# Optimization experiments

Measured on AMD Instinct MI355X. Metric: run time of the kernel, lower is better.

## Reference

```python
import jax, jax.numpy as jnp
import numpy as np

EMBED = 1024
HEADS = 16
HEAD_DIM = EMBED // HEADS
SCALE = HEAD_DIM ** (-0.5)
LN_EPS = 1e-5


def setup_inputs() -> dict:
    key = jax.random.key(0)
    ks = jax.random.split(key, 8)
    B, N = 2, 2048
    s = EMBED ** -0.5
    return {
        "x": jax.random.normal(ks[0], (B, N, EMBED), dtype=jnp.float32),
        "ln_w": jnp.ones((EMBED,), jnp.float32),
        "ln_b": jnp.zeros((EMBED,), jnp.float32),
        "Wq": jax.random.normal(ks[1], (EMBED, EMBED), jnp.float32) * s,
        "Wk": jax.random.normal(ks[2], (EMBED, EMBED), jnp.float32) * s,
        "Wv": jax.random.normal(ks[3], (EMBED, EMBED), jnp.float32) * s,
        "Wo": jax.random.normal(ks[4], (EMBED, EMBED), jnp.float32) * s,
        "bo": jnp.zeros((EMBED,), jnp.float32),
    }


def reference(x, ln_w, ln_b, Wq, Wk, Wv, Wo, bo):
    residual = x
    # LayerNorm (pre-norm)
    mu = jnp.mean(x, axis=-1, keepdims=True)
    var = jnp.mean(jnp.square(x - mu), axis=-1, keepdims=True)
    xn = (x - mu) * jax.lax.rsqrt(var + LN_EPS) * ln_w + ln_b

    B, N, _ = xn.shape
    q = (xn @ Wq.T).reshape(B, N, HEADS, HEAD_DIM).transpose(0, 2, 1, 3)  # b h n d
    k = (xn @ Wk.T).reshape(B, N, HEADS, HEAD_DIM).transpose(0, 2, 1, 3)
    v = (xn @ Wv.T).reshape(B, N, HEADS, HEAD_DIM).transpose(0, 2, 1, 3)

    dots = jnp.einsum('bhqd,bhkd->bhqk', q, k) * SCALE
    causal = jnp.tril(jnp.ones((N, N), dtype=bool))
    dots = jnp.where(causal, dots, -jnp.inf)
    attn = jax.nn.softmax(dots, axis=-1)
    out = jnp.einsum('bhqk,bhkd->bhqd', attn, v)
    out = out.transpose(0, 2, 1, 3).reshape(B, N, EMBED)
    # dropout is identity in eval mode
    return residual + out @ Wo.T + bo
```

## Files before the change

### kernel.cpp

```cpp
#include <hip/hip_runtime.h>

#define E 1024
#define NSEQ 2048
#define HEADS 16
#define HD 64

typedef unsigned short u16;
typedef short short8 __attribute__((ext_vector_type(8)));
typedef float f32x4 __attribute__((ext_vector_type(4)));

template<bool B> struct BC { static constexpr bool v = B; };

#define GLOAD_LDS16(gp, lp)                                        \
    __builtin_amdgcn_global_load_lds(                              \
        (const __attribute__((address_space(1))) void*)(gp),       \
        (__attribute__((address_space(3))) void*)(lp), 16, 0, 0)

__device__ __forceinline__ u16 f2bf(float f) {
    union { float f; unsigned u; } v; v.f = f;
    unsigned r = v.u + 0x7fffu + ((v.u >> 16) & 1u);
    return (u16)(r >> 16);
}

__device__ __forceinline__ unsigned cvt_pk_bf16(float lo, float hi) {
    unsigned r;
    asm("v_cvt_pk_bf16_f32 %0, %1, %2" : "=v"(r) : "v"(lo), "v"(hi));
    return r;
}

__device__ __forceinline__ f32x4 mfma16(short8 a, short8 b, f32x4 c) {
    return __builtin_amdgcn_mfma_f32_16x16x32_bf16(a, b, c, 0, 0, 0);
}

__global__ __launch_bounds__(256) void convw_k(
    const float* __restrict__ Wq, const float* __restrict__ Wk,
    const float* __restrict__ Wv, const float* __restrict__ Wo,
    u16* __restrict__ out)
{
    const unsigned i = (blockIdx.x * 256u + threadIdx.x) * 4u;
    const unsigned m = i >> 20;
    const float* src = (m == 0) ? Wq : (m == 1) ? Wk : (m == 2) ? Wv : Wo;
    const float4 v = *(const float4*)(src + (i & 0xFFFFFu));
    *(uint2*)(out + i) = make_uint2(
        ((unsigned)f2bf(v.x)) | (((unsigned)f2bf(v.y)) << 16),
        ((unsigned)f2bf(v.z)) | (((unsigned)f2bf(v.w)) << 16));
}

__global__ __launch_bounds__(256) void ln_fwd(
    const float* __restrict__ X, const float* __restrict__ w,
    const float* __restrict__ bb, u16* __restrict__ xn)
{
    const int row = blockIdx.x, tid = threadIdx.x;
    const int lane = tid & 63, wave = tid >> 6;
    const float4 v = ((const float4*)(X + (size_t)row * E))[tid];
    float s = v.x + v.y + v.z + v.w;
    float s2 = v.x * v.x + v.y * v.y + v.z * v.z + v.w * v.w;
#pragma unroll
    for (int off = 1; off < 64; off <<= 1) {
        s += __shfl_xor(s, off);
        s2 += __shfl_xor(s2, off);
    }
    __shared__ float red[8];
    if (lane == 0) { red[wave] = s; red[4 + wave] = s2; }
    __syncthreads();
    s = red[0] + red[1] + red[2] + red[3];
    s2 = red[4] + red[5] + red[6] + red[7];
    const float mu = s * (1.f / 1024.f);
    float var = s2 * (1.f / 1024.f) - mu * mu;
    var = fmaxf(var, 0.f);
    const float rs = rsqrtf(var + 1e-5f);
    const float4 wv = ((const float4*)w)[tid];
    const float4 bv = ((const float4*)bb)[tid];
    u16 o0 = f2bf((v.x - mu) * rs * wv.x + bv.x);
    u16 o1 = f2bf((v.y - mu) * rs * wv.y + bv.y);
    u16 o2 = f2bf((v.z - mu) * rs * wv.z + bv.z);
    u16 o3 = f2bf((v.w - mu) * rs * wv.w + bv.w);
    *(uint2*)(xn + (size_t)row * E + tid * 4) =
        make_uint2(((unsigned)o0) | (((unsigned)o1) << 16),
                   ((unsigned)o2) | (((unsigned)o3) << 16));
}

__global__ __launch_bounds__(256) void vtrans(
    const u16* __restrict__ Vb, u16* __restrict__ VT)
{
    __shared__ u16 tl[64][65];
    const int t = threadIdx.x;
    const int ntile = blockIdx.x, bh = blockIdx.y;
    const int b = bh >> 4, h = bh & 15;
    const int n0 = ntile * 64;
    {
        const int nl = t >> 2;
        const u16* src = Vb + ((size_t)b * NSEQ + n0 + nl) * E + h * 64;
#pragma unroll
        for (int u = 0; u < 2; ++u) {
            const int d0 = (t & 3) * 16 + u * 8;
            short8 v = *(const short8*)(src + d0);
#pragma unroll
            for (int j = 0; j < 8; ++j) tl[nl][d0 + j] = (u16)v[j];
        }
    }
    __syncthreads();
    {
        const int d = t >> 2, nc = (t & 3) * 16;
        u16* dst = VT + ((size_t)bh * 64 + d) * NSEQ + n0 + nc;
#pragma unroll
        for (int u = 0; u < 2; ++u) {
            short8 o;
#pragma unroll
            for (int j = 0; j < 8; ++j) o[j] = (short)tl[nc + u * 8 + j][d];
            *(short8*)(dst + u * 8) = o;
        }
    }
}

template<int MODE>
__global__ __launch_bounds__(256) void gemm_nt(
    const u16* __restrict__ A, const u16* __restrict__ Wbase,
    u16* __restrict__ outb, float* __restrict__ outf,
    const float* __restrict__ resid, const float* __restrict__ bias)
{
    __shared__ __align__(16) unsigned char As[128 * 128];
    __shared__ __align__(16) unsigned char Bs[128 * 128];
    const int tid = threadIdx.x;
    const int lane = tid & 63, wave = tid >> 6;
    const int l15 = lane & 15, l4 = lane >> 4;
    const int wm = wave >> 1, wn = wave & 1;
    const int nt = blockIdx.x, mt = blockIdx.y, z = blockIdx.z;
    const u16* Bw = Wbase + (size_t)z * (E * (size_t)E);

    const int lrow8 = lane >> 3;
    const int lchunk = (lane & 7) ^ lrow8;
    const u16* gA = A + (size_t)(mt * 128 + lrow8) * E + lchunk * 8;
    const u16* gB = Bw + (size_t)(nt * 128 + lrow8) * E + lchunk * 8;

    f32x4 acc[4][4] = {};

    for (int kt = 0; kt < 16; ++kt) {
#pragma unroll
        for (int i = 0; i < 4; ++i) {
            const int rb = (i * 4 + wave) * 8;
            GLOAD_LDS16(gA + (size_t)rb * E + kt * 64, As + rb * 128);
            GLOAD_LDS16(gB + (size_t)rb * E + kt * 64, Bs + rb * 128);
        }
        __syncthreads();
#pragma unroll
        for (int ks = 0; ks < 2; ++ks) {
            short8 af[4], bfr[4];
#pragma unroll
            for (int i = 0; i < 4; ++i) {
                int ra = wm * 64 + i * 16 + l15;
                af[i] = *(const short8*)(As + ra * 128 + ((ks * 64 + l4 * 16) ^ ((ra & 7) << 4)));
                int rb2 = wn * 64 + i * 16 + l15;
                bfr[i] = *(const short8*)(Bs + rb2 * 128 + ((ks * 64 + l4 * 16) ^ ((rb2 & 7) << 4)));
            }
#pragma unroll
            for (int i = 0; i < 4; ++i)
#pragma unroll
                for (int j = 0; j < 4; ++j)
                    acc[i][j] = mfma16(af[i], bfr[j], acc[i][j]);
        }
        __syncthreads();
    }

    const int orow0 = mt * 128 + wm * 64, ocol0 = nt * 128 + wn * 64;
    if (MODE == 0) {
        u16* outz = outb + (size_t)z * (4096 * (size_t)E);
        const float osc = (z == 0) ? 0.18033688f : 1.0f;
#pragma unroll
        for (int i = 0; i < 4; ++i)
#pragma unroll
            for (int j = 0; j < 4; ++j)
#pragma unroll
                for (int r = 0; r < 4; ++r) {
                    int row = orow0 + i * 16 + l4 * 4 + r;
                    int col = ocol0 + j * 16 + l15;
                    outz[(size_t)row * E + col] = f2bf(acc[i][j][r] * osc);
                }
    } else {
#pragma unroll
        for (int i = 0; i < 4; ++i)
#pragma unroll
            for (int j = 0; j < 4; ++j)
#pragma unroll
                for (int r = 0; r < 4; ++r) {
                    int row = orow0 + i * 16 + l4 * 4 + r;
                    int col = ocol0 + j * 16 + l15;
                    size_t idx = (size_t)row * E + col;
                    outf[idx] = acc[i][j][r] + resid[idx] + bias[col];
                }
    }
}

__global__ __launch_bounds__(256) void attn_fwd(
    const u16* __restrict__ Q, const u16* __restrict__ K,
    const u16* __restrict__ VT, u16* __restrict__ O)
{
    __shared__ __align__(16) unsigned char Kls[2 * 16384];
    __shared__ __align__(16) unsigned char Vls[2 * 16384];
    __shared__ __align__(16) unsigned char Ps[4 * 4096];
    const int tid = threadIdx.x, lane = tid & 63, wave = tid >> 6;
    const int sub = wave >> 1, par = wave & 1;
    const int l15 = lane & 15, l4 = lane >> 4;
    const int h = blockIdx.x, j = blockIdx.y, b = blockIdx.z;
    const size_t bbase = (size_t)b * NSEQ * E + h * HD;
    const u16* vt = VT + ((size_t)(b * 16 + h) * 64) * NSEQ;

    unsigned char* Pw = Ps + wave * 4096;
    const int srowK = lane >> 3, kchunk = (lane & 7) ^ srowK;
    const int srowV = lane >> 4, vchunk = (lane & 15) ^ (((wave & 1) << 2) + srowV);

    auto stage = [&](int t, int buf) {
        const u16* Kg = K + bbase + (size_t)(t * 128) * E;
        const u16* vg = vt + t * 128;
        unsigned char* kd = Kls + buf * 16384 + wave * 1024;
        unsigned char* vd = Vls + buf * 16384 + wave * 1024;
#pragma unroll
        for (int i = 0; i < 4; ++i)
            GLOAD_LDS16(Kg + (size_t)(wave * 8 + i * 32 + srowK) * E + kchunk * 8, kd + i * 4096);
#pragma unroll
        for (int i = 0; i < 4; ++i)
            GLOAD_LDS16(vg + (size_t)(wave * 4 + i * 16 + srowV) * NSEQ + vchunk * 8, vd + i * 4096);
    };

    auto run_strip = [&](int jj) {
        const int qw0 = jj * 64 + sub * 32;
        const int R = (jj >> 1) + 1;

        short8 aq[2][2];
#pragma unroll
        for (int qt = 0; qt < 2; ++qt)
#pragma unroll
            for (int ks = 0; ks < 2; ++ks)
                aq[qt][ks] = *(const short8*)(Q + bbase + (size_t)(qw0 + qt * 16 + l15) * E + ks * 32 + l4 * 8);

        f32x4 accO[2][4] = {};
        float mrow[2] = {-5e29f, -5e29f};
        float lrow[2] = {0.f, 0.f};

        stage(0, 0);
        __syncthreads();

        auto step = [&](int t, auto mc) {
            constexpr bool MASK = decltype(mc)::v;
            const int buf = t & 1;
            if (t + 1 < R) stage(t + 1, buf ^ 1);
            const unsigned char* Kc = Kls + buf * 16384;
            const unsigned char* Vc = Vls + buf * 16384;

            f32x4 s[2][4] = {};
#pragma unroll
            for (int kvt = 0; kvt < 4; ++kvt) {
                const int kr = par * 64 + kvt * 16 + l15;
#pragma unroll
                for (int ks = 0; ks < 2; ++ks) {
                    short8 kfr = *(const short8*)(Kc + kr * 128 + ((ks * 64 + l4 * 16) ^ ((kr & 7) << 4)));
                    s[0][kvt] = mfma16(kfr, aq[0][ks], s[0][kvt]);
                    s[1][kvt] = mfma16(kfr, aq[1][ks], s[1][kvt]);
                }
            }

            if constexpr (MASK) {
#pragma unroll
                for (int qt = 0; qt < 2; ++qt) {
                    const int qg = qw0 + qt * 16 + l15;
#pragma unroll
                    for (int kvt = 0; kvt < 4; ++kvt)
#pragma unroll
                        for (int r = 0; r < 4; ++r) {
                            int kvg = t * 128 + par * 64 + kvt * 16 + l4 * 4 + r;
                            if (kvg > qg) s[qt][kvt][r] = -1e30f;
                        }
                }
            }

#pragma unroll
            for (int qt = 0; qt < 2; ++qt) {
                float m0 = fmaxf(fmaxf(s[qt][0][0], s[qt][0][1]), fmaxf(s[qt][0][2], s[qt][0][3]));
                float m1 = fmaxf(fmaxf(s[qt][1][0], s[qt][1][1]), fmaxf(s[qt][1][2], s[qt][1][3]));
                float m2 = fmaxf(fmaxf(s[qt][2][0], s[qt][2][1]), fmaxf(s[qt][2][2], s[qt][2][3]));
                float m3 = fmaxf(fmaxf(s[qt][3][0], s[qt][3][1]), fmaxf(s[qt][3][2], s[qt][3][3]));
                float pm = fmaxf(fmaxf(m0, m1), fmaxf(m2, m3));
                if (__any(pm > mrow[qt] + 8.f)) {
                    pm = fmaxf(pm, __shfl_xor(pm, 16));
                    pm = fmaxf(pm, __shfl_xor(pm, 32));
                    const float mn = fmaxf(mrow[qt], pm);
                    const float sc = exp2f(mrow[qt] - mn);
                    mrow[qt] = mn;
                    lrow[qt] *= sc;
#pragma unroll
                    for (int r = 0; r < 4; ++r) {
                        float scv = __shfl(sc, l4 * 4 + r);
#pragma unroll
                        for (int dt = 0; dt < 4; ++dt) accO[qt][dt][r] *= scv;
                    }
                }
                const int pr = qt * 16 + l15;
                const int sw = (l15 & 7) << 4;
#pragma unroll
                for (int kvt = 0; kvt < 4; ++kvt) {
                    float p0 = exp2f(s[qt][kvt][0] - mrow[qt]);
                    float p1 = exp2f(s[qt][kvt][1] - mrow[qt]);
                    float p2 = exp2f(s[qt][kvt][2] - mrow[qt]);
                    float p3 = exp2f(s[qt][kvt][3] - mrow[qt]);
                    lrow[qt] += (p0 + p1) + (p2 + p3);
                    uint2 pk = make_uint2(cvt_pk_bf16(p0, p1), cvt_pk_bf16(p2, p3));
                    *(uint2*)(Pw + pr * 128 + ((kvt * 32 + l4 * 8) ^ sw)) = pk;
                }
            }

#pragma unroll
            for (int ks2 = 0; ks2 < 2; ++ks2) {
                const int cb = ks2 * 64 + l4 * 16;
                short8 pf0 = *(const short8*)(Pw + l15 * 128 + (cb ^ ((l15 & 7) << 4)));
                short8 pf1 = *(const short8*)(Pw + (16 + l15) * 128 + (cb ^ ((l15 & 7) << 4)));
#pragma unroll
                for (int dt = 0; dt < 4; ++dt) {
                    const int vr = dt * 16 + l15;
                    short8 vfr = *(const short8*)(Vc + vr * 256 + ((par * 128 + cb) ^ ((vr & 7) << 4)));
                    accO[0][dt] = mfma16(pf0, vfr, accO[0][dt]);
                    accO[1][dt] = mfma16(pf1, vfr, accO[1][dt]);
                }
            }
            __syncthreads();
        };

        for (int t = 0; t + 1 < R; ++t) step(t, BC<false>{});
        step(R - 1, BC<true>{});

        f32x4* Mg = (f32x4*)Kls;
        if (par == 1) {
            f32x4 hd;
            hd[0] = mrow[0]; hd[1] = mrow[1]; hd[2] = lrow[0]; hd[3] = lrow[1];
            Mg[(sub * 9) * 64 + lane] = hd;
#pragma unroll
            for (int qt = 0; qt < 2; ++qt)
#pragma unroll
                for (int dt = 0; dt < 4; ++dt)
                    Mg[(sub * 9 + 1 + qt * 4 + dt) * 64 + lane] = accO[qt][dt];
        }
        __syncthreads();
        if (par == 0) {
            f32x4 hd = Mg[(sub * 9) * 64 + lane];
            float scA[2], scB[2];
#pragma unroll
            for (int qt = 0; qt < 2; ++qt) {
                const float mB = hd[qt], lB = hd[2 + qt];
                const float ms = fmaxf(mrow[qt], mB);
                scA[qt] = exp2f(mrow[qt] - ms);
                scB[qt] = exp2f(mB - ms);
                lrow[qt] = lrow[qt] * scA[qt] + lB * scB[qt];
            }
#pragma unroll
            for (int qt = 0; qt < 2; ++qt)
#pragma unroll
                for (int r = 0; r < 4; ++r) {
                    float sa = __shfl(scA[qt], l4 * 4 + r);
                    float sb = __shfl(scB[qt], l4 * 4 + r);
#pragma unroll
                    for (int dt = 0; dt < 4; ++dt) {
                        f32x4 ob = Mg[(sub * 9 + 1 + qt * 4 + dt) * 64 + lane];
                        accO[qt][dt][r] = accO[qt][dt][r] * sa + ob[r] * sb;
                    }
                }
            float linv[2];
#pragma unroll
            for (int qt = 0; qt < 2; ++qt) {
                float tl2 = lrow[qt];
                tl2 += __shfl_xor(tl2, 16);
                tl2 += __shfl_xor(tl2, 32);
                linv[qt] = 1.f / tl2;
            }
#pragma unroll
            for (int rt = 0; rt < 2; ++rt)
#pragma unroll
                for (int r = 0; r < 4; ++r) {
                    float lq = __shfl(linv[rt], l4 * 4 + r);
                    const int qg = qw0 + rt * 16 + l4 * 4 + r;
#pragma unroll
                    for (int dt = 0; dt < 4; ++dt)
                        O[bbase + (size_t)qg * E + dt * 16 + l15] = f2bf(accO[rt][dt][r] * lq);
                }
        }
        __syncthreads();
    };

    run_strip(j);
    run_strip(31 - j);
}

extern "C" void kernel_launch(void* const* d_in, const int* in_sizes, int n_in,
                              void* d_out, int out_size, void* d_ws, size_t ws_size,
                              hipStream_t stream)
{
    const float* x    = (const float*)d_in[0];
    const float* ln_w = (const float*)d_in[1];
    const float* ln_b = (const float*)d_in[2];
    const float* Wq   = (const float*)d_in[3];
    const float* Wk   = (const float*)d_in[4];
    const float* Wv   = (const float*)d_in[5];
    const float* Wo   = (const float*)d_in[6];
    const float* bo   = (const float*)d_in[7];
    float* out = (float*)d_out;

    u16* ws  = (u16*)d_ws;
    u16* Wbf = ws;
    u16* xn  = Wbf + (size_t)4 * 1024 * 1024;
    u16* Qb  = xn + (size_t)4096 * 1024;
    u16* Kb  = Qb + (size_t)4096 * 1024;
    u16* Vb  = Kb + (size_t)4096 * 1024;
    u16* Ob  = Vb + (size_t)4096 * 1024;
    u16* VT  = xn;

    convw_k<<<dim3(4096), dim3(256), 0, stream>>>(Wq, Wk, Wv, Wo, Wbf);
    ln_fwd<<<dim3(4096), dim3(256), 0, stream>>>(x, ln_w, ln_b, xn);
    gemm_nt<0><<<dim3(8, 32, 3), dim3(256), 0, stream>>>(
        xn, Wbf, Qb, nullptr, nullptr, nullptr);
    vtrans<<<dim3(32, 32), dim3(256), 0, stream>>>(Vb, VT);
    attn_fwd<<<dim3(16, 16, 2), dim3(256), 0, stream>>>(Qb, Kb, VT, Ob);
    gemm_nt<1><<<dim3(8, 32, 1), dim3(256), 0, stream>>>(
        Ob, Wbf + (size_t)3 * 1024 * 1024, nullptr, out, x, bo);
}
```

Baseline: 122.4 us.

## Load V fragments directly from global into registers, drop V LDS staging

The attention kernel no longer stages V^T tiles through shared memory. Each wave loads its own V fragments straight from global memory into registers, prefetching the next tile after the PV MFMAs. LDS address offsets are precomputed once per thread, and s_setprio is raised around the MFMA blocks. This halves LDS footprint and removes the V LDS traffic, but exposes global load latency on V loads that are only one step ahead, and adds register pressure.

```diff
diff --git a/kernel.cpp b/kernel.cpp
--- a/kernel.cpp
+++ b/kernel.cpp
@@ -196,30 +196,53 @@
     const u16* __restrict__ VT, u16* __restrict__ O)
 {
     __shared__ __align__(16) unsigned char Kls[2 * 16384];
-    __shared__ __align__(16) unsigned char Vls[2 * 16384];
     __shared__ __align__(16) unsigned char Ps[4 * 4096];
     const int tid = threadIdx.x, lane = tid & 63, wave = tid >> 6;
     const int sub = wave >> 1, par = wave & 1;
     const int l15 = lane & 15, l4 = lane >> 4;
-    const int h = blockIdx.x, j = blockIdx.y, b = blockIdx.z;
+    const int h = blockIdx.x, jg = blockIdx.y, b = blockIdx.z;
     const size_t bbase = (size_t)b * NSEQ * E + h * HD;
     const u16* vt = VT + ((size_t)(b * 16 + h) * 64) * NSEQ;
 
     unsigned char* Pw = Ps + wave * 4096;
     const int srowK = lane >> 3, kchunk = (lane & 7) ^ srowK;
-    const int srowV = lane >> 4, vchunk = (lane & 15) ^ (((wave & 1) << 2) + srowV);
+
+    int koff[4][2];
+#pragma unroll
+    for (int kvt = 0; kvt < 4; ++kvt) {
+        const int kr = par * 64 + kvt * 16 + l15;
+#pragma unroll
+        for (int ks = 0; ks < 2; ++ks)
+            koff[kvt][ks] = kr * 128 + ((ks * 64 + l4 * 16) ^ ((kr & 7) << 4));
+    }
+    int pwo[2][4];
+#pragma unroll
+    for (int qt = 0; qt < 2; ++qt) {
+        const int pr = qt * 16 + l15;
+#pragma unroll
+        for (int kvt = 0; kvt < 4; ++kvt)
+            pwo[qt][kvt] = pr * 128 + ((kvt * 32 + l4 * 8) ^ ((l15 & 7) << 4));
+    }
+    int pro[2][2];
+#pragma unroll
+    for (int ks2 = 0; ks2 < 2; ++ks2) {
+        const int cb = (ks2 * 64 + l4 * 16) ^ ((l15 & 7) << 4);
+        pro[ks2][0] = l15 * 128 + cb;
+        pro[ks2][1] = (16 + l15) * 128 + cb;
+    }
+    int vgo[2][4];
+#pragma unroll
+    for (int ks2 = 0; ks2 < 2; ++ks2)
+#pragma unroll
+        for (int dt = 0; dt < 4; ++dt)
+            vgo[ks2][dt] = (dt * 16 + l15) * NSEQ + par * 64 + ks2 * 32 + l4 * 8;
 
     auto stage = [&](int t, int buf) {
         const u16* Kg = K + bbase + (size_t)(t * 128) * E;
-        const u16* vg = vt + t * 128;
         unsigned char* kd = Kls + buf * 16384 + wave * 1024;
-        unsigned char* vd = Vls + buf * 16384 + wave * 1024;
 #pragma unroll
         for (int i = 0; i < 4; ++i)
             GLOAD_LDS16(Kg + (size_t)(wave * 8 + i * 32 + srowK) * E + kchunk * 8, kd + i * 4096);
-#pragma unroll
-        for (int i = 0; i < 4; ++i)
-            GLOAD_LDS16(vg + (size_t)(wave * 4 + i * 16 + srowV) * NSEQ + vchunk * 8, vd + i * 4096);
     };
 
     auto run_strip = [&](int jj) {
@@ -236,6 +259,13 @@
         f32x4 accO[2][4] = {};
         float mrow[2] = {-5e29f, -5e29f};
         float lrow[2] = {0.f, 0.f};
+
+        short8 vf[2][4];
+#pragma unroll
+        for (int ks2 = 0; ks2 < 2; ++ks2)
+#pragma unroll
+            for (int dt = 0; dt < 4; ++dt)
+                vf[ks2][dt] = *(const short8*)(vt + vgo[ks2][dt]);
 
         stage(0, 0);
         __syncthreads();
@@ -245,19 +275,18 @@
             const int buf = t & 1;
             if (t + 1 < R) stage(t + 1, buf ^ 1);
             const unsigned char* Kc = Kls + buf * 16384;
-            const unsigned char* Vc = Vls + buf * 16384;
 
             f32x4 s[2][4] = {};
-#pragma unroll
-            for (int kvt = 0; kvt < 4; ++kvt) {
-                const int kr = par * 64 + kvt * 16 + l15;
+            __builtin_amdgcn_s_setprio(1);
+#pragma unroll
+            for (int kvt = 0; kvt < 4; ++kvt)
 #pragma unroll
                 for (int ks = 0; ks < 2; ++ks) {
-                    short8 kfr = *(const short8*)(Kc + kr * 128 + ((ks * 64 + l4 * 16) ^ ((kr & 7) << 4)));
+                    short8 kfr = *(const short8*)(Kc + koff[kvt][ks]);
                     s[0][kvt] = mfma16(kfr, aq[0][ks], s[0][kvt]);
                     s[1][kvt] = mfma16(kfr, aq[1][ks], s[1][kvt]);
                 }
-            }
+            __builtin_amdgcn_s_setprio(0);
 
             if constexpr (MASK) {
 #pragma unroll
@@ -294,8 +323,6 @@
                         for (int dt = 0; dt < 4; ++dt) accO[qt][dt][r] *= scv;
                     }
                 }
-                const int pr = qt * 16 + l15;
-                const int sw = (l15 & 7) << 4;
 #pragma unroll
                 for (int kvt = 0; kvt < 4; ++kvt) {
                     float p0 = exp2f(s[qt][kvt][0] - mrow[qt]);
@@ -304,22 +331,30 @@
                     float p3 = exp2f(s[qt][kvt][3] - mrow[qt]);
                     lrow[qt] += (p0 + p1) + (p2 + p3);
                     uint2 pk = make_uint2(cvt_pk_bf16(p0, p1), cvt_pk_bf16(p2, p3));
-                    *(uint2*)(Pw + pr * 128 + ((kvt * 32 + l4 * 8) ^ sw)) = pk;
-                }
-            }
-
+                    *(uint2*)(Pw + pwo[qt][kvt]) = pk;
+                }
+            }
+
+            __builtin_amdgcn_s_setprio(1);
 #pragma unroll
             for (int ks2 = 0; ks2 < 2; ++ks2) {
-                const int cb = ks2 * 64 + l4 * 16;
-                short8 pf0 = *(const short8*)(Pw + l15 * 128 + (cb ^ ((l15 & 7) << 4)));
-                short8 pf1 = *(const short8*)(Pw + (16 + l15) * 128 + (cb ^ ((l15 & 7) << 4)));
+                short8 pf0 = *(const short8*)(Pw + pro[ks2][0]);
+                short8 pf1 = *(const short8*)(Pw + pro[ks2][1]);
 #pragma unroll
                 for (int dt = 0; dt < 4; ++dt) {
-                    const int vr = dt * 16 + l15;
-                    short8 vfr = *(const short8*)(Vc + vr * 256 + ((par * 128 + cb) ^ ((vr & 7) << 4)));
-                    accO[0][dt] = mfma16(pf0, vfr, accO[0][dt]);
-                    accO[1][dt] = mfma16(pf1, vfr, accO[1][dt]);
-                }
+                    accO[0][dt] = mfma16(pf0, vf[ks2][dt], accO[0][dt]);
+                    accO[1][dt] = mfma16(pf1, vf[ks2][dt], accO[1][dt]);
+                }
+            }
+            __builtin_amdgcn_s_setprio(0);
+
+            if (t + 1 < R) {
+                const u16* vg = vt + (t + 1) * 128;
+#pragma unroll
+                for (int ks2 = 0; ks2 < 2; ++ks2)
+#pragma unroll
+                    for (int dt = 0; dt < 4; ++dt)
+                        vf[ks2][dt] = *(const short8*)(vg + vgo[ks2][dt]);
             }
             __syncthreads();
         };
@@ -384,8 +419,8 @@
         __syncthreads();
     };
 
-    run_strip(j);
-    run_strip(31 - j);
+    run_strip(jg);
+    run_strip(31 - jg);
 }
 
 extern "C" void kernel_launch(void* const* d_in, const int* in_sizes, int n_in,
```

Result: slower. 126.6 us (+3.5%).
